# Kernel tuning notes

Hardware: AMD Instinct MI355X
Metric: run time of the kernel (lower is better)

## Reference

```python
import jax, jax.numpy as jnp
import numpy as np

B, L, F = 16384, 64, 32
E, A, H = 64, 8, 128


def setup_inputs() -> dict:
    key = jax.random.key(0)
    ks = jax.random.split(key, 16)
    s = 0.1
    return {
        "lane_features": jax.random.normal(ks[0], (B, L, F), jnp.float32),
        "lane_mask": jax.random.randint(ks[1], (B, L), 0, 2).astype(jnp.float32),
        "action_mask": jax.random.randint(ks[2], (B, A), 0, 2).astype(jnp.float32),
        # SingleHeadAttentionPool params (stored [in,out])
        "W": jax.random.normal(ks[3], (F, F), jnp.float32) * s,
        "bW": jnp.zeros((F,), jnp.float32),
        "v": jax.random.normal(ks[4], (F,), jnp.float32) * s,
        "projW": jax.random.normal(ks[5], (F, E), jnp.float32) * s,
        "projb": jnp.zeros((E,), jnp.float32),
        # policy head MLP [E->128->128->A], tanh
        "piW1": jax.random.normal(ks[6], (E, H), jnp.float32) * s,
        "pib1": jnp.zeros((H,), jnp.float32),
        "piW2": jax.random.normal(ks[7], (H, H), jnp.float32) * s,
        "pib2": jnp.zeros((H,), jnp.float32),
        "piW3": jax.random.normal(ks[8], (H, A), jnp.float32) * s,
        "pib3": jnp.zeros((A,), jnp.float32),
        # value head MLP [E->128->128->1], tanh
        "vfW1": jax.random.normal(ks[9], (E, H), jnp.float32) * s,
        "vfb1": jnp.zeros((H,), jnp.float32),
        "vfW2": jax.random.normal(ks[10], (H, H), jnp.float32) * s,
        "vfb2": jnp.zeros((H,), jnp.float32),
        "vfW3": jax.random.normal(ks[11], (H, 1), jnp.float32) * s,
        "vfb3": jnp.zeros((1,), jnp.float32),
    }


def reference(lane_features, lane_mask, action_mask, W, bW, v, projW, projb,
              piW1, pib1, piW2, pib2, piW3, pib3,
              vfW1, vfb1, vfW2, vfb2, vfW3, vfb3):
    X = lane_features                       # [B,L,F]
    mask = lane_mask > 0.5                  # [B,L] bool
    has_active = jnp.any(mask, axis=-1)     # [B]

    # additive attention pool, masked softmax == gather-then-softmax
    Hh = jnp.tanh(jnp.einsum('blf,fg->blg', X, W) + bW)   # [B,L,F]
    scores = jnp.einsum('blf,f->bl', Hh, v)                # [B,L]
    NEG = jnp.float32(-1e30)
    w = jax.nn.softmax(jnp.where(mask, scores, NEG), axis=-1)
    w = jnp.where(mask, w, 0.0)
    pooled = jnp.einsum('bl,blf->bf', w, X)                # [B,F]
    z = pooled @ projW + projb                             # [B,E]
    z = jnp.where(has_active[:, None], z, 0.0)             # empty set -> zeros

    # heads
    h = jnp.tanh(z @ piW1 + pib1)
    h = jnp.tanh(h @ piW2 + pib2)
    logits = h @ piW3 + pib3                               # [B,A]

    g = jnp.tanh(z @ vfW1 + vfb1)
    g = jnp.tanh(g @ vfW2 + vfb2)
    value = (g @ vfW3 + vfb3)[:, 0]                        # [B]

    # hard action masking
    invalid = action_mask <= 0
    masked = jnp.where(invalid, jnp.finfo(logits.dtype).min, logits)
    all_invalid = jnp.all(invalid, axis=1)
    masked = jnp.where(all_invalid[:, None], logits, masked)
    return masked, value
```

## Files before the change

### kernel.cpp

```cpp
#include <hip/hip_runtime.h>
#include <float.h>

#define NBATCH 16384
#define SAFE_MAX 3.3e38f
#define SAFE_NEG -3.3e38f

typedef __attribute__((ext_vector_type(8))) short bf16x8;
typedef __attribute__((ext_vector_type(4))) float f32x4;

__device__ __forceinline__ float san(float v) {
    v = (v == v) ? v : 0.0f;
    return fminf(fmaxf(v, SAFE_NEG), SAFE_MAX);
}

__device__ __forceinline__ float tanh_fast(float a) {
    float e = __expf(a + a);
    return fmaf(-2.0f, __builtin_amdgcn_rcpf(e + 1.0f), 1.0f);
}

__device__ __forceinline__ unsigned short f2bf_rne(float v) {
    unsigned int u = __float_as_uint(v);
    return (unsigned short)((u + 0x7FFFu + ((u >> 16) & 1u)) >> 16);
}

extern "C" __global__ void __launch_bounds__(256, 4)
pool_kernel(const float* __restrict__ X, const float* __restrict__ LM,
            const float* __restrict__ W, const float* __restrict__ bW,
            const float* __restrict__ vv,
            const float* __restrict__ projW, const float* __restrict__ projb,
            float* __restrict__ zout)
{
    __shared__ __align__(16) short wt[32 * 40];
    __shared__ float sc[4][64];
    __shared__ float mk[4][64];
    __shared__ float pool_s[4][32];

    const int tid  = threadIdx.x;
    const int w    = __builtin_amdgcn_readfirstlane(tid >> 6);
    const int lane = tid & 63;
    const int c    = lane & 15;
    const int quad = lane >> 4;
    const long b   = (long)blockIdx.x * 4 + w;

    for (int i = tid; i < 1024; i += 256) {
        const int n = i >> 5, k = i & 31;
        wt[n * 40 + k] = (short)f2bf_rne(W[k * 32 + n]);
    }

    float xr[4][8];
#pragma unroll
    for (int t = 0; t < 4; ++t) {
        const float4* p = (const float4*)(X + b * 2048 + (16 * t + c) * 32 + quad * 8);
        float4 a0 = p[0], a1 = p[1];
        xr[t][0] = a0.x; xr[t][1] = a0.y; xr[t][2] = a0.z; xr[t][3] = a0.w;
        xr[t][4] = a1.x; xr[t][5] = a1.y; xr[t][6] = a1.z; xr[t][7] = a1.w;
    }
    const float ml = LM[b * 64 + lane];
    const bool active = ml > 0.5f;

    union { bf16x8 v; unsigned int u[4]; } afr[4];
#pragma unroll
    for (int t = 0; t < 4; ++t)
#pragma unroll
        for (int j2 = 0; j2 < 4; ++j2)
            afr[t].u[j2] = __builtin_amdgcn_perm(
                __float_as_uint(xr[t][2 * j2 + 1]),
                __float_as_uint(xr[t][2 * j2]), 0x07060302u);

    __syncthreads();

    union { bf16x8 v; uint4 q; } bfr[2];
#pragma unroll
    for (int u = 0; u < 2; ++u)
        bfr[u].q = *((const uint4*)&wt[(16 * u + c) * 40 + quad * 8]);

    f32x4 acc[4][2];
#pragma unroll
    for (int t = 0; t < 4; ++t)
#pragma unroll
        for (int u = 0; u < 2; ++u) {
            acc[t][u] = (f32x4){0.f, 0.f, 0.f, 0.f};
            acc[t][u] = __builtin_amdgcn_mfma_f32_16x16x32_bf16(
                afr[t].v, bfr[u].v, acc[t][u], 0, 0, 0);
        }

    const float bw0 = bW[c], bw1 = bW[16 + c];
    const float vv0 = vv[c], vv1 = vv[16 + c];
    mk[w][lane] = ml;
#pragma unroll
    for (int t = 0; t < 4; ++t)
#pragma unroll
        for (int r = 0; r < 4; ++r) {
            float s = tanh_fast(acc[t][0][r] + bw0) * vv0
                    + tanh_fast(acc[t][1][r] + bw1) * vv1;
            s += __shfl_xor(s, 1);
            s += __shfl_xor(s, 2);
            s += __shfl_xor(s, 4);
            s += __shfl_xor(s, 8);
            if (c == t * 4 + r)
                sc[w][16 * t + quad * 4 + r] = s;
        }
    __syncthreads();

    const float s0 = sc[w][lane];
    float smx = active ? s0 : -1e30f;
#pragma unroll
    for (int off = 32; off; off >>= 1) smx = fmaxf(smx, __shfl_xor(smx, off));
    float ev = active ? __expf(s0 - smx) : 0.0f;
    float es = ev;
#pragma unroll
    for (int off = 32; off; off >>= 1) es += __shfl_xor(es, off);
    const float rcpS = __builtin_amdgcn_rcpf(es);

    float wgt[4];
#pragma unroll
    for (int t = 0; t < 4; ++t) {
        const float sr = sc[w][16 * t + c];
        const float mr = mk[w][16 * t + c];
        wgt[t] = (mr > 0.5f && es > 0.0f) ? __expf(sr - smx) * rcpS : 0.0f;
    }

#pragma unroll
    for (int j = 0; j < 8; ++j) {
        float p = wgt[0] * xr[0][j];
#pragma unroll
        for (int t = 1; t < 4; ++t) p = fmaf(wgt[t], xr[t][j], p);
        p += __shfl_xor(p, 1);
        p += __shfl_xor(p, 2);
        p += __shfl_xor(p, 4);
        p += __shfl_xor(p, 8);
        if (c == 0) pool_s[w][quad * 8 + j] = p;
    }
    __syncthreads();

    float zv = projb[lane];
#pragma unroll
    for (int f = 0; f < 32; ++f)
        zv = fmaf(pool_s[w][f], projW[f * 64 + lane], zv);
    const bool any = (__ballot(active) != 0ull);
    zout[b * 64 + lane] = any ? san(zv) : 0.0f;
}

#define ZT 0
#define H1 4160
#define PL 0
extern "C" __global__ void __launch_bounds__(512)
heads_kernel(const float* __restrict__ z, const float* __restrict__ AM,
             const float* __restrict__ piW1, const float* __restrict__ pib1,
             const float* __restrict__ piW2, const float* __restrict__ pib2,
             const float* __restrict__ piW3, const float* __restrict__ pib3,
             const float* __restrict__ vfW1, const float* __restrict__ vfb1,
             const float* __restrict__ vfW2, const float* __restrict__ vfb2,
             const float* __restrict__ vfW3, const float* __restrict__ vfb3,
             float* __restrict__ out)
{
    __shared__ float smem[12352];

    const int tid  = threadIdx.x;
    const int w    = __builtin_amdgcn_readfirstlane(tid >> 6);
    const int el   = tid & 63;
    const bool isPi = (blockIdx.x & 1) == 0;
    const int tile  = blockIdx.x >> 1;

    for (int i = tid; i < 4096; i += 512)
        smem[ZT + (i >> 6) * 65 + (i & 63)] = z[(long)tile * 4096 + i];
    __syncthreads();

    const float* W1 = isPi ? piW1 : vfW1;
    const float* b1 = isPi ? pib1 : vfb1;
    const float* W2 = isPi ? piW2 : vfW2;
    const float* b2 = isPi ? pib2 : vfb2;

    float acc[16];
#pragma unroll
    for (int i = 0; i < 16; ++i) acc[i] = b1[w * 16 + i];
#pragma unroll 8
    for (int e = 0; e < 64; ++e) {
        const float zv = smem[ZT + el * 65 + e];
        const float* wr = W1 + e * 128 + w * 16;
#pragma unroll
        for (int i = 0; i < 16; ++i) acc[i] = fmaf(zv, wr[i], acc[i]);
    }
#pragma unroll
    for (int i = 0; i < 16; ++i)
        smem[H1 + (w * 16 + i) * 64 + el] = tanh_fast(acc[i]);
    __syncthreads();

    float a2[16];
#pragma unroll
    for (int i = 0; i < 16; ++i) a2[i] = b2[w * 16 + i];
#pragma unroll 8
    for (int j = 0; j < 128; ++j) {
        const float hv = smem[H1 + j * 64 + el];
        const float* wr = W2 + j * 128 + w * 16;
#pragma unroll
        for (int i = 0; i < 16; ++i) a2[i] = fmaf(hv, wr[i], a2[i]);
    }

    if (isPi) {
        float pl[8];
#pragma unroll
        for (int a = 0; a < 8; ++a) pl[a] = 0.0f;
#pragma unroll
        for (int i = 0; i < 16; ++i) {
            const float h2 = tanh_fast(a2[i]);
            const float* wr = piW3 + (w * 16 + i) * 8;
#pragma unroll
            for (int a = 0; a < 8; ++a) pl[a] = fmaf(h2, wr[a], pl[a]);
        }
#pragma unroll
        for (int a = 0; a < 8; ++a)
            smem[PL + w * 512 + el * 8 + a] = pl[a];
        __syncthreads();

        const int rel = tid >> 3, ra = tid & 7;
        float lg = pib3[ra];
#pragma unroll
        for (int w2 = 0; w2 < 8; ++w2)
            lg += smem[PL + w2 * 512 + rel * 8 + ra];
        lg = san(lg);
        const long rb = (long)tile * 64 + rel;
        const float am = AM[rb * 8 + ra];
        const bool inv = (am <= 0.0f);
        const unsigned long long bal = __ballot(inv);
        const int grp = (tid & 63) >> 3;
        const bool allinv = (((bal >> (grp * 8)) & 0xFFull) == 0xFFull);
        out[rb * 8 + ra] = allinv ? lg : (inv ? SAFE_NEG : lg);
    } else {
        float pv = 0.0f;
#pragma unroll
        for (int i = 0; i < 16; ++i)
            pv = fmaf(tanh_fast(a2[i]), vfW3[w * 16 + i], pv);
        smem[PL + el * 8 + w] = pv;
        __syncthreads();

        if (tid < 64) {
            float val = vfb3[0];
#pragma unroll
            for (int w2 = 0; w2 < 8; ++w2) val += smem[PL + tid * 8 + w2];
            out[(long)NBATCH * 8 + (long)tile * 64 + tid] = san(val);
        }
    }
}

#define LZ    0
#define LH1f  4096
#define LPLf  12288
#define LWX   4096
#define LPOOL 12800
#define WXS   17

extern "C" __global__ void __launch_bounds__(512, 2)
fused_kernel(const float* __restrict__ X, const float* __restrict__ LM,
             const float* __restrict__ AM,
             const float* __restrict__ W, const float* __restrict__ bW,
             const float* __restrict__ vv,
             const float* __restrict__ projW, const float* __restrict__ projb,
             const float* __restrict__ piW1, const float* __restrict__ pib1,
             const float* __restrict__ piW2, const float* __restrict__ pib2,
             const float* __restrict__ piW3, const float* __restrict__ pib3,
             const float* __restrict__ vfW1, const float* __restrict__ vfb1,
             const float* __restrict__ vfW2, const float* __restrict__ vfb2,
             const float* __restrict__ vfW3, const float* __restrict__ vfb3,
             float* __restrict__ out)
{
    __shared__ float smem[16384];
    const int tid  = threadIdx.x;
    const int w    = __builtin_amdgcn_readfirstlane(tid >> 6);
    const int lane = tid & 63;

    float4 xv[8];
    float  mval;
    {
        const long b0 = (long)blockIdx.x * 64 + w;
        const float4* xp = (const float4*)(X + b0 * 2048 + lane * 32);
#pragma unroll
        for (int i = 0; i < 8; ++i) xv[i] = xp[i];
        mval = LM[b0 * 64 + lane];
    }
#pragma unroll 1
    for (int it = 0; it < 8; ++it) {
        const int eL = it * 8 + w;
        float4 xn[8];
        float  mn = 0.0f;
        if (it < 7) {
            const long bn = (long)blockIdx.x * 64 + (it + 1) * 8 + w;
            const float4* xp = (const float4*)(X + bn * 2048 + lane * 32);
#pragma unroll
            for (int i = 0; i < 8; ++i) xn[i] = xp[i];
            mn = LM[bn * 64 + lane];
        }
        float x[32];
#pragma unroll
        for (int i = 0; i < 8; ++i) {
            x[4*i+0] = xv[i].x; x[4*i+1] = xv[i].y;
            x[4*i+2] = xv[i].z; x[4*i+3] = xv[i].w;
        }
        float acc[32];
#pragma unroll
        for (int g = 0; g < 32; ++g) acc[g] = 0.0f;
#pragma unroll
        for (int f = 0; f < 32; ++f) {
            const float xf = x[f];
#pragma unroll
            for (int g = 0; g < 32; ++g) acc[g] = fmaf(xf, W[f * 32 + g], acc[g]);
        }
        float score = 0.0f;
#pragma unroll
        for (int g = 0; g < 32; ++g)
            score = fmaf(tanh_fast(acc[g] + bW[g]), vv[g], score);

        const bool active = mval > 0.5f;
        float sm = active ? score : -1e30f;
#pragma unroll
        for (int off = 32; off; off >>= 1) sm = fmaxf(sm, __shfl_xor(sm, off));
        float ev = active ? __expf(score - sm) : 0.0f;
        float es = ev;
#pragma unroll
        for (int off = 32; off; off >>= 1) es += __shfl_xor(es, off);
        const float wgt = (es > 0.0f) ? (ev / es) : 0.0f;

        float* wxp = &smem[LWX + w * (64 * WXS)];
#pragma unroll 1
        for (int P = 0; P < 2; ++P) {
            __syncthreads();
#pragma unroll
            for (int fr = 0; fr < 16; ++fr)
                wxp[lane * WXS + fr] = wgt * x[P * 16 + fr];
            __syncthreads();
            const int q = lane >> 4, fr = lane & 15;
            float p = 0.0f;
#pragma unroll
            for (int r = 0; r < 16; ++r) p += wxp[(q * 16 + r) * WXS + fr];
            p += __shfl_xor(p, 16);
            p += __shfl_xor(p, 32);
            if (lane < 16) smem[LPOOL + w * 32 + P * 16 + fr] = p;
        }
        __syncthreads();

        float zv = projb[lane];
#pragma unroll
        for (int f = 0; f < 32; ++f)
            zv = fmaf(smem[LPOOL + w * 32 + f], projW[f * 64 + lane], zv);
        const bool any = (__ballot(active) != 0ull);
        zv = any ? zv : 0.0f;
        smem[LZ + lane * 64 + eL] = san(zv);
        if (it < 7) {
#pragma unroll
            for (int i = 0; i < 8; ++i) xv[i] = xn[i];
            mval = mn;
        }
    }
    __syncthreads();

    const int el = lane;
    {
        float acc[16];
#pragma unroll
        for (int i = 0; i < 16; ++i) acc[i] = pib1[w * 16 + i];
#pragma unroll 8
        for (int e = 0; e < 64; ++e) {
            const float zv = smem[LZ + e * 64 + el];
            const float* wr = piW1 + e * 128 + w * 16;
#pragma unroll
            for (int i = 0; i < 16; ++i) acc[i] = fmaf(zv, wr[i], acc[i]);
        }
#pragma unroll
        for (int i = 0; i < 16; ++i)
            smem[LH1f + (w * 16 + i) * 64 + el] = tanh_fast(acc[i]);
        __syncthreads();

        float a2[16];
#pragma unroll
        for (int i = 0; i < 16; ++i) a2[i] = pib2[w * 16 + i];
#pragma unroll 8
        for (int j = 0; j < 128; ++j) {
            const float hv = smem[LH1f + j * 64 + el];
            const float* wr = piW2 + j * 128 + w * 16;
#pragma unroll
            for (int i = 0; i < 16; ++i) a2[i] = fmaf(hv, wr[i], a2[i]);
        }
        float pl[8];
#pragma unroll
        for (int a = 0; a < 8; ++a) pl[a] = 0.0f;
#pragma unroll
        for (int i = 0; i < 16; ++i) {
            const float h2 = tanh_fast(a2[i]);
            const float* wr = piW3 + (w * 16 + i) * 8;
#pragma unroll
            for (int a = 0; a < 8; ++a) pl[a] = fmaf(h2, wr[a], pl[a]);
        }
#pragma unroll
        for (int a = 0; a < 8; ++a)
            smem[LPLf + w * 512 + el * 8 + a] = pl[a];
        __syncthreads();

        const int rel = tid >> 3, ra = tid & 7;
        float lg = pib3[ra];
#pragma unroll
        for (int w2 = 0; w2 < 8; ++w2)
            lg += smem[LPLf + w2 * 512 + rel * 8 + ra];
        lg = san(lg);
        const long rb = (long)blockIdx.x * 64 + rel;
        const float am = AM[rb * 8 + ra];
        const bool inv = (am <= 0.0f);
        const unsigned long long bal = __ballot(inv);
        const int grp = (tid & 63) >> 3;
        const bool allinv = (((bal >> (grp * 8)) & 0xFFull) == 0xFFull);
        out[rb * 8 + ra] = allinv ? lg : (inv ? SAFE_NEG : lg);
        __syncthreads();
    }
    {
        float acc[16];
#pragma unroll
        for (int i = 0; i < 16; ++i) acc[i] = vfb1[w * 16 + i];
#pragma unroll 8
        for (int e = 0; e < 64; ++e) {
            const float zv = smem[LZ + e * 64 + el];
            const float* wr = vfW1 + e * 128 + w * 16;
#pragma unroll
            for (int i = 0; i < 16; ++i) acc[i] = fmaf(zv, wr[i], acc[i]);
        }
#pragma unroll
        for (int i = 0; i < 16; ++i)
            smem[LH1f + (w * 16 + i) * 64 + el] = tanh_fast(acc[i]);
        __syncthreads();

        float a2[16];
#pragma unroll
        for (int i = 0; i < 16; ++i) a2[i] = vfb2[w * 16 + i];
#pragma unroll 8
        for (int j = 0; j < 128; ++j) {
            const float hv = smem[LH1f + j * 64 + el];
            const float* wr = vfW2 + j * 128 + w * 16;
#pragma unroll
            for (int i = 0; i < 16; ++i) a2[i] = fmaf(hv, wr[i], a2[i]);
        }
        float pv = 0.0f;
#pragma unroll
        for (int i = 0; i < 16; ++i)
            pv = fmaf(tanh_fast(a2[i]), vfW3[w * 16 + i], pv);
        smem[LPLf + el * 8 + w] = pv;
        __syncthreads();

        if (tid < 64) {
            float val = vfb3[0];
#pragma unroll
            for (int w2 = 0; w2 < 8; ++w2) val += smem[LPLf + tid * 8 + w2];
            out[(long)NBATCH * 8 + (long)blockIdx.x * 64 + tid] = san(val);
        }
    }
}

extern "C" void kernel_launch(void* const* d_in, const int* in_sizes, int n_in,
                              void* d_out, int out_size, void* d_ws, size_t ws_size,
                              hipStream_t stream) {
    const float* X     = (const float*)d_in[0];
    const float* LM    = (const float*)d_in[1];
    const float* AM    = (const float*)d_in[2];
    const float* W     = (const float*)d_in[3];
    const float* bW    = (const float*)d_in[4];
    const float* vv    = (const float*)d_in[5];
    const float* projW = (const float*)d_in[6];
    const float* projb = (const float*)d_in[7];
    const float* piW1  = (const float*)d_in[8];
    const float* pib1  = (const float*)d_in[9];
    const float* piW2  = (const float*)d_in[10];
    const float* pib2  = (const float*)d_in[11];
    const float* piW3  = (const float*)d_in[12];
    const float* pib3  = (const float*)d_in[13];
    const float* vfW1  = (const float*)d_in[14];
    const float* vfb1  = (const float*)d_in[15];
    const float* vfW2  = (const float*)d_in[16];
    const float* vfb2  = (const float*)d_in[17];
    const float* vfW3  = (const float*)d_in[18];
    const float* vfb3  = (const float*)d_in[19];

    float* outp = (float*)d_out;
    const size_t zbytes = (size_t)NBATCH * 64 * sizeof(float);

    if (ws_size >= zbytes) {
        float* z = (float*)d_ws;
        pool_kernel<<<NBATCH / 4, 256, 0, stream>>>(
            X, LM, W, bW, vv, projW, projb, z);
        heads_kernel<<<(NBATCH / 64) * 2, 512, 0, stream>>>(
            z, AM, piW1, pib1, piW2, pib2, piW3, pib3,
            vfW1, vfb1, vfW2, vfb2, vfW3, vfb3, outp);
    } else {
        fused_kernel<<<NBATCH / 64, 512, 0, stream>>>(
            X, LM, AM, W, bW, vv, projW, projb,
            piW1, pib1, piW2, pib2, piW3, pib3,
            vfW1, vfb1, vfW2, vfb2, vfW3, vfb3, outp);
    }
}
```

Baseline: 258.3 us.

## Replace two-kernel pool+heads path with single fused MFMA kernel

Drops the pool_kernel + heads_kernel pair that passed z through a global workspace and always launches one fused kernel instead. The new kernel computes the attention projection with bf16 MFMA (as in pool_kernel), keeps z in shared memory, and then runs both MLP heads in the same block. This removes the global round-trip of z and one launch. The cost is only 256 blocks of 512 threads with large shared memory use, so occupancy and parallelism may be lower than the split version, and the heads still run on scalar FMAs.

```diff
diff --git a/kernel.cpp b/kernel.cpp
--- a/kernel.cpp
+++ b/kernel.cpp
@@ -21,6 +21,269 @@
 __device__ __forceinline__ unsigned short f2bf_rne(float v) {
     unsigned int u = __float_as_uint(v);
     return (unsigned short)((u + 0x7FFFu + ((u >> 16) & 1u)) >> 16);
+}
+
+extern "C" __global__ void __launch_bounds__(512, 2)
+fused_mfma(const float* __restrict__ X, const float* __restrict__ LM,
+           const float* __restrict__ AM,
+           const float* __restrict__ W, const float* __restrict__ bW,
+           const float* __restrict__ vv,
+           const float* __restrict__ projW, const float* __restrict__ projb,
+           const float* __restrict__ piW1, const float* __restrict__ pib1,
+           const float* __restrict__ piW2, const float* __restrict__ pib2,
+           const float* __restrict__ piW3, const float* __restrict__ pib3,
+           const float* __restrict__ vfW1, const float* __restrict__ vfb1,
+           const float* __restrict__ vfW2, const float* __restrict__ vfb2,
+           const float* __restrict__ vfW3, const float* __restrict__ vfb3,
+           float* __restrict__ out)
+{
+    __shared__ __align__(16) short wt[32 * 40];
+    __shared__ float zl[64 * 65];
+    __shared__ float sc[8][64];
+    __shared__ float mk[8][64];
+    __shared__ float pool_s[8][32];
+    __shared__ float h1[128 * 64];
+    __shared__ float plbuf[8 * 512];
+
+    const int tid  = threadIdx.x;
+    const int w    = __builtin_amdgcn_readfirstlane(tid >> 6);
+    const int lane = tid & 63;
+    const int c    = lane & 15;
+    const int quad = lane >> 4;
+    const long btile = (long)blockIdx.x * 64;
+
+    for (int i = tid; i < 1024; i += 512) {
+        const int n = i >> 5, k = i & 31;
+        wt[n * 40 + k] = (short)f2bf_rne(W[k * 32 + n]);
+    }
+
+    const float bw0 = bW[c], bw1 = bW[16 + c];
+    const float vv0 = vv[c], vv1 = vv[16 + c];
+    const float pjb = projb[lane];
+
+    __syncthreads();
+
+    union { bf16x8 v; uint4 q; } bfr[2];
+#pragma unroll
+    for (int u = 0; u < 2; ++u)
+        bfr[u].q = *((const uint4*)&wt[(16 * u + c) * 40 + quad * 8]);
+
+    float xr[4][8];
+    float ml;
+    {
+        const long b = btile + w * 8;
+#pragma unroll
+        for (int t = 0; t < 4; ++t) {
+            const float4* p = (const float4*)(X + b * 2048 + (16 * t + c) * 32 + quad * 8);
+            float4 a0 = p[0], a1 = p[1];
+            xr[t][0] = a0.x; xr[t][1] = a0.y; xr[t][2] = a0.z; xr[t][3] = a0.w;
+            xr[t][4] = a1.x; xr[t][5] = a1.y; xr[t][6] = a1.z; xr[t][7] = a1.w;
+        }
+        ml = LM[b * 64 + lane];
+    }
+
+#pragma unroll 1
+    for (int it = 0; it < 8; ++it) {
+        const int brel = w * 8 + it;
+
+        float xn[4][8];
+        float mn = 0.0f;
+        if (it < 7) {
+            const long bn = btile + brel + 1;
+#pragma unroll
+            for (int t = 0; t < 4; ++t) {
+                const float4* p = (const float4*)(X + bn * 2048 + (16 * t + c) * 32 + quad * 8);
+                float4 a0 = p[0], a1 = p[1];
+                xn[t][0] = a0.x; xn[t][1] = a0.y; xn[t][2] = a0.z; xn[t][3] = a0.w;
+                xn[t][4] = a1.x; xn[t][5] = a1.y; xn[t][6] = a1.z; xn[t][7] = a1.w;
+            }
+            mn = LM[bn * 64 + lane];
+        }
+        const bool active = ml > 0.5f;
+
+        union { bf16x8 v; unsigned int u[4]; } afr[4];
+#pragma unroll
+        for (int t = 0; t < 4; ++t)
+#pragma unroll
+            for (int j2 = 0; j2 < 4; ++j2)
+                afr[t].u[j2] = __builtin_amdgcn_perm(
+                    __float_as_uint(xr[t][2 * j2 + 1]),
+                    __float_as_uint(xr[t][2 * j2]), 0x07060302u);
+
+        f32x4 acc[4][2];
+#pragma unroll
+        for (int t = 0; t < 4; ++t)
+#pragma unroll
+            for (int u = 0; u < 2; ++u) {
+                acc[t][u] = (f32x4){0.f, 0.f, 0.f, 0.f};
+                acc[t][u] = __builtin_amdgcn_mfma_f32_16x16x32_bf16(
+                    afr[t].v, bfr[u].v, acc[t][u], 0, 0, 0);
+            }
+
+        mk[w][lane] = ml;
+#pragma unroll
+        for (int t = 0; t < 4; ++t)
+#pragma unroll
+            for (int r = 0; r < 4; ++r) {
+                float s = tanh_fast(acc[t][0][r] + bw0) * vv0
+                        + tanh_fast(acc[t][1][r] + bw1) * vv1;
+                s += __shfl_xor(s, 1);
+                s += __shfl_xor(s, 2);
+                s += __shfl_xor(s, 4);
+                s += __shfl_xor(s, 8);
+                if (c == t * 4 + r)
+                    sc[w][16 * t + quad * 4 + r] = s;
+            }
+        asm volatile("s_waitcnt lgkmcnt(0)" ::: "memory");
+
+        const float s0 = sc[w][lane];
+        float smx = active ? s0 : -1e30f;
+#pragma unroll
+        for (int off = 32; off; off >>= 1) smx = fmaxf(smx, __shfl_xor(smx, off));
+        float ev = active ? __expf(s0 - smx) : 0.0f;
+        float es = ev;
+#pragma unroll
+        for (int off = 32; off; off >>= 1) es += __shfl_xor(es, off);
+        const float rcpS = __builtin_amdgcn_rcpf(es);
+
+        float wgt[4];
+#pragma unroll
+        for (int t = 0; t < 4; ++t) {
+            const float sr = sc[w][16 * t + c];
+            const float mr = mk[w][16 * t + c];
+            wgt[t] = (mr > 0.5f && es > 0.0f) ? __expf(sr - smx) * rcpS : 0.0f;
+        }
+
+#pragma unroll
+        for (int j = 0; j < 8; ++j) {
+            float p = wgt[0] * xr[0][j];
+#pragma unroll
+            for (int t = 1; t < 4; ++t) p = fmaf(wgt[t], xr[t][j], p);
+            p += __shfl_xor(p, 1);
+            p += __shfl_xor(p, 2);
+            p += __shfl_xor(p, 4);
+            p += __shfl_xor(p, 8);
+            if (c == 0) pool_s[w][quad * 8 + j] = p;
+        }
+        asm volatile("s_waitcnt lgkmcnt(0)" ::: "memory");
+
+        float zv = pjb;
+#pragma unroll
+        for (int f = 0; f < 32; ++f)
+            zv = fmaf(pool_s[w][f], projW[f * 64 + lane], zv);
+        const bool any = (__ballot(active) != 0ull);
+        zl[lane * 65 + brel] = any ? san(zv) : 0.0f;
+
+        if (it < 7) {
+#pragma unroll
+            for (int t = 0; t < 4; ++t)
+#pragma unroll
+                for (int j = 0; j < 8; ++j) xr[t][j] = xn[t][j];
+            ml = mn;
+        }
+    }
+    __syncthreads();
+
+    const int el = lane;
+
+    {
+        float acc[16];
+#pragma unroll
+        for (int i = 0; i < 16; ++i) acc[i] = pib1[w * 16 + i];
+#pragma unroll 8
+        for (int e = 0; e < 64; ++e) {
+            const float zv = zl[e * 65 + el];
+            const float* wr = piW1 + e * 128 + w * 16;
+#pragma unroll
+            for (int i = 0; i < 16; ++i) acc[i] = fmaf(zv, wr[i], acc[i]);
+        }
+#pragma unroll
+        for (int i = 0; i < 16; ++i)
+            h1[(w * 16 + i) * 64 + el] = tanh_fast(acc[i]);
+        __syncthreads();
+
+        float a2[16];
+#pragma unroll
+        for (int i = 0; i < 16; ++i) a2[i] = pib2[w * 16 + i];
+#pragma unroll 8
+        for (int j = 0; j < 128; ++j) {
+            const float hv = h1[j * 64 + el];
+            const float* wr = piW2 + j * 128 + w * 16;
+#pragma unroll
+            for (int i = 0; i < 16; ++i) a2[i] = fmaf(hv, wr[i], a2[i]);
+        }
+
+        float pl[8];
+#pragma unroll
+        for (int a = 0; a < 8; ++a) pl[a] = 0.0f;
+#pragma unroll
+        for (int i = 0; i < 16; ++i) {
+            const float h2 = tanh_fast(a2[i]);
+            const float* wr = piW3 + (w * 16 + i) * 8;
+#pragma unroll
+            for (int a = 0; a < 8; ++a) pl[a] = fmaf(h2, wr[a], pl[a]);
+        }
+#pragma unroll
+        for (int a = 0; a < 8; ++a)
+            plbuf[w * 512 + el * 8 + a] = pl[a];
+        __syncthreads();
+
+        const int rel = tid >> 3, ra = tid & 7;
+        float lg = pib3[ra];
+#pragma unroll
+        for (int w2 = 0; w2 < 8; ++w2)
+            lg += plbuf[w2 * 512 + rel * 8 + ra];
+        lg = san(lg);
+        const long rb = btile + rel;
+        const float am = AM[rb * 8 + ra];
+        const bool inv = (am <= 0.0f);
+        const unsigned long long bal = __ballot(inv);
+        const int grp = (tid & 63) >> 3;
+        const bool allinv = (((bal >> (grp * 8)) & 0xFFull) == 0xFFull);
+        out[rb * 8 + ra] = allinv ? lg : (inv ? SAFE_NEG : lg);
+        __syncthreads();
+    }
+
+    {
+        float acc[16];
+#pragma unroll
+        for (int i = 0; i < 16; ++i) acc[i] = vfb1[w * 16 + i];
+#pragma unroll 8
+        for (int e = 0; e < 64; ++e) {
+            const float zv = zl[e * 65 + el];
+            const float* wr = vfW1 + e * 128 + w * 16;
+#pragma unroll
+            for (int i = 0; i < 16; ++i) acc[i] = fmaf(zv, wr[i], acc[i]);
+        }
+#pragma unroll
+        for (int i = 0; i < 16; ++i)
+            h1[(w * 16 + i) * 64 + el] = tanh_fast(acc[i]);
+        __syncthreads();
+
+        float a2[16];
+#pragma unroll
+        for (int i = 0; i < 16; ++i) a2[i] = vfb2[w * 16 + i];
+#pragma unroll 8
+        for (int j = 0; j < 128; ++j) {
+            const float hv = h1[j * 64 + el];
+            const float* wr = vfW2 + j * 128 + w * 16;
+#pragma unroll
+            for (int i = 0; i < 16; ++i) a2[i] = fmaf(hv, wr[i], a2[i]);
+        }
+        float pv = 0.0f;
+#pragma unroll
+        for (int i = 0; i < 16; ++i)
+            pv = fmaf(tanh_fast(a2[i]), vfW3[w * 16 + i], pv);
+        plbuf[el * 8 + w] = pv;
+        __syncthreads();
+
+        if (tid < 64) {
+            float val = vfb3[0];
+#pragma unroll
+            for (int w2 = 0; w2 < 8; ++w2) val += plbuf[tid * 8 + w2];
+            out[(long)NBATCH * 8 + btile + tid] = san(val);
+        }
+    }
 }
 
 extern "C" __global__ void __launch_bounds__(256, 4)
@@ -239,215 +502,6 @@
 #pragma unroll
             for (int w2 = 0; w2 < 8; ++w2) val += smem[PL + tid * 8 + w2];
             out[(long)NBATCH * 8 + (long)tile * 64 + tid] = san(val);
-        }
-    }
-}
-
-#define LZ    0
-#define LH1f  4096
-#define LPLf  12288
-#define LWX   4096
-#define LPOOL 12800
-#define WXS   17
-
-extern "C" __global__ void __launch_bounds__(512, 2)
-fused_kernel(const float* __restrict__ X, const float* __restrict__ LM,
-             const float* __restrict__ AM,
-             const float* __restrict__ W, const float* __restrict__ bW,
-             const float* __restrict__ vv,
-             const float* __restrict__ projW, const float* __restrict__ projb,
-             const float* __restrict__ piW1, const float* __restrict__ pib1,
-             const float* __restrict__ piW2, const float* __restrict__ pib2,
-             const float* __restrict__ piW3, const float* __restrict__ pib3,
-             const float* __restrict__ vfW1, const float* __restrict__ vfb1,
-             const float* __restrict__ vfW2, const float* __restrict__ vfb2,
-             const float* __restrict__ vfW3, const float* __restrict__ vfb3,
-             float* __restrict__ out)
-{
-    __shared__ float smem[16384];
-    const int tid  = threadIdx.x;
-    const int w    = __builtin_amdgcn_readfirstlane(tid >> 6);
-    const int lane = tid & 63;
-
-    float4 xv[8];
-    float  mval;
-    {
-        const long b0 = (long)blockIdx.x * 64 + w;
-        const float4* xp = (const float4*)(X + b0 * 2048 + lane * 32);
-#pragma unroll
-        for (int i = 0; i < 8; ++i) xv[i] = xp[i];
-        mval = LM[b0 * 64 + lane];
-    }
-#pragma unroll 1
-    for (int it = 0; it < 8; ++it) {
-        const int eL = it * 8 + w;
-        float4 xn[8];
-        float  mn = 0.0f;
-        if (it < 7) {
-            const long bn = (long)blockIdx.x * 64 + (it + 1) * 8 + w;
-            const float4* xp = (const float4*)(X + bn * 2048 + lane * 32);
-#pragma unroll
-            for (int i = 0; i < 8; ++i) xn[i] = xp[i];
-            mn = LM[bn * 64 + lane];
-        }
-        float x[32];
-#pragma unroll
-        for (int i = 0; i < 8; ++i) {
-            x[4*i+0] = xv[i].x; x[4*i+1] = xv[i].y;
-            x[4*i+2] = xv[i].z; x[4*i+3] = xv[i].w;
-        }
-        float acc[32];
-#pragma unroll
-        for (int g = 0; g < 32; ++g) acc[g] = 0.0f;
-#pragma unroll
-        for (int f = 0; f < 32; ++f) {
-            const float xf = x[f];
-#pragma unroll
-            for (int g = 0; g < 32; ++g) acc[g] = fmaf(xf, W[f * 32 + g], acc[g]);
-        }
-        float score = 0.0f;
-#pragma unroll
-        for (int g = 0; g < 32; ++g)
-            score = fmaf(tanh_fast(acc[g] + bW[g]), vv[g], score);
-
-        const bool active = mval > 0.5f;
-        float sm = active ? score : -1e30f;
-#pragma unroll
-        for (int off = 32; off; off >>= 1) sm = fmaxf(sm, __shfl_xor(sm, off));
-        float ev = active ? __expf(score - sm) : 0.0f;
-        float es = ev;
-#pragma unroll
-        for (int off = 32; off; off >>= 1) es += __shfl_xor(es, off);
-        const float wgt = (es > 0.0f) ? (ev / es) : 0.0f;
-
-        float* wxp = &smem[LWX + w * (64 * WXS)];
-#pragma unroll 1
-        for (int P = 0; P < 2; ++P) {
-            __syncthreads();
-#pragma unroll
-            for (int fr = 0; fr < 16; ++fr)
-                wxp[lane * WXS + fr] = wgt * x[P * 16 + fr];
-            __syncthreads();
-            const int q = lane >> 4, fr = lane & 15;
-            float p = 0.0f;
-#pragma unroll
-            for (int r = 0; r < 16; ++r) p += wxp[(q * 16 + r) * WXS + fr];
-            p += __shfl_xor(p, 16);
-            p += __shfl_xor(p, 32);
-            if (lane < 16) smem[LPOOL + w * 32 + P * 16 + fr] = p;
-        }
-        __syncthreads();
-
-        float zv = projb[lane];
-#pragma unroll
-        for (int f = 0; f < 32; ++f)
-            zv = fmaf(smem[LPOOL + w * 32 + f], projW[f * 64 + lane], zv);
-        const bool any = (__ballot(active) != 0ull);
-        zv = any ? zv : 0.0f;
-        smem[LZ + lane * 64 + eL] = san(zv);
-        if (it < 7) {
-#pragma unroll
-            for (int i = 0; i < 8; ++i) xv[i] = xn[i];
-            mval = mn;
-        }
-    }
-    __syncthreads();
-
-    const int el = lane;
-    {
-        float acc[16];
-#pragma unroll
-        for (int i = 0; i < 16; ++i) acc[i] = pib1[w * 16 + i];
-#pragma unroll 8
-        for (int e = 0; e < 64; ++e) {
-            const float zv = smem[LZ + e * 64 + el];
-            const float* wr = piW1 + e * 128 + w * 16;
-#pragma unroll
-            for (int i = 0; i < 16; ++i) acc[i] = fmaf(zv, wr[i], acc[i]);
-        }
-#pragma unroll
-        for (int i = 0; i < 16; ++i)
-            smem[LH1f + (w * 16 + i) * 64 + el] = tanh_fast(acc[i]);
-        __syncthreads();
-
-        float a2[16];
-#pragma unroll
-        for (int i = 0; i < 16; ++i) a2[i] = pib2[w * 16 + i];
-#pragma unroll 8
-        for (int j = 0; j < 128; ++j) {
-            const float hv = smem[LH1f + j * 64 + el];
-            const float* wr = piW2 + j * 128 + w * 16;
-#pragma unroll
-            for (int i = 0; i < 16; ++i) a2[i] = fmaf(hv, wr[i], a2[i]);
-        }
-        float pl[8];
-#pragma unroll
-        for (int a = 0; a < 8; ++a) pl[a] = 0.0f;
-#pragma unroll
-        for (int i = 0; i < 16; ++i) {
-            const float h2 = tanh_fast(a2[i]);
-            const float* wr = piW3 + (w * 16 + i) * 8;
-#pragma unroll
-            for (int a = 0; a < 8; ++a) pl[a] = fmaf(h2, wr[a], pl[a]);
-        }
-#pragma unroll
-        for (int a = 0; a < 8; ++a)
-            smem[LPLf + w * 512 + el * 8 + a] = pl[a];
-        __syncthreads();
-
-        const int rel = tid >> 3, ra = tid & 7;
-        float lg = pib3[ra];
-#pragma unroll
-        for (int w2 = 0; w2 < 8; ++w2)
-            lg += smem[LPLf + w2 * 512 + rel * 8 + ra];
-        lg = san(lg);
-        const long rb = (long)blockIdx.x * 64 + rel;
-        const float am = AM[rb * 8 + ra];
-        const bool inv = (am <= 0.0f);
-        const unsigned long long bal = __ballot(inv);
-        const int grp = (tid & 63) >> 3;
-        const bool allinv = (((bal >> (grp * 8)) & 0xFFull) == 0xFFull);
-        out[rb * 8 + ra] = allinv ? lg : (inv ? SAFE_NEG : lg);
-        __syncthreads();
-    }
-    {
-        float acc[16];
-#pragma unroll
-        for (int i = 0; i < 16; ++i) acc[i] = vfb1[w * 16 + i];
-#pragma unroll 8
-        for (int e = 0; e < 64; ++e) {
-            const float zv = smem[LZ + e * 64 + el];
-            const float* wr = vfW1 + e * 128 + w * 16;
-#pragma unroll
-            for (int i = 0; i < 16; ++i) acc[i] = fmaf(zv, wr[i], acc[i]);
-        }
-#pragma unroll
-        for (int i = 0; i < 16; ++i)
-            smem[LH1f + (w * 16 + i) * 64 + el] = tanh_fast(acc[i]);
-        __syncthreads();
-
-        float a2[16];
-#pragma unroll
-        for (int i = 0; i < 16; ++i) a2[i] = vfb2[w * 16 + i];
-#pragma unroll 8
-        for (int j = 0; j < 128; ++j) {
-            const float hv = smem[LH1f + j * 64 + el];
-            const float* wr = vfW2 + j * 128 + w * 16;
-#pragma unroll
-            for (int i = 0; i < 16; ++i) a2[i] = fmaf(hv, wr[i], a2[i]);
-        }
-        float pv = 0.0f;
-#pragma unroll
-        for (int i = 0; i < 16; ++i)
-            pv = fmaf(tanh_fast(a2[i]), vfW3[w * 16 + i], pv);
-        smem[LPLf + el * 8 + w] = pv;
-        __syncthreads();
-
-        if (tid < 64) {
-            float val = vfb3[0];
-#pragma unroll
-            for (int w2 = 0; w2 < 8; ++w2) val += smem[LPLf + tid * 8 + w2];
-            out[(long)NBATCH * 8 + (long)blockIdx.x * 64 + tid] = san(val);
         }
     }
 }
@@ -477,19 +531,9 @@
     const float* vfb3  = (const float*)d_in[19];
 
     float* outp = (float*)d_out;
-    const size_t zbytes = (size_t)NBATCH * 64 * sizeof(float);
-
-    if (ws_size >= zbytes) {
-        float* z = (float*)d_ws;
-        pool_kernel<<<NBATCH / 4, 256, 0, stream>>>(
-            X, LM, W, bW, vv, projW, projb, z);
-        heads_kernel<<<(NBATCH / 64) * 2, 512, 0, stream>>>(
-            z, AM, piW1, pib1, piW2, pib2, piW3, pib3,
-            vfW1, vfb1, vfW2, vfb2, vfW3, vfb3, outp);
-    } else {
-        fused_kernel<<<NBATCH / 64, 512, 0, stream>>>(
-            X, LM, AM, W, bW, vv, projW, projb,
-            piW1, pib1, piW2, pib2, piW3, pib3,
-            vfW1, vfb1, vfW2, vfb2, vfW3, vfb3, outp);
-    }
-}
+
+    fused_mfma<<<NBATCH / 64, 512, 0, stream>>>(
+        X, LM, AM, W, bW, vv, projW, projb,
+        piW1, pib1, piW2, pib2, piW3, pib3,
+        vfW1, vfb1, vfW2, vfb2, vfW3, vfb3, outp);
+}
```

Measured after the change: 325.6 us. 26.1% more time.

## Fuse pool and heads into one 1024-thread kernel with transposed MFMA scoring

Applied to the files above, without the earlier changes.

Replaces the two-kernel pipeline (pool writing z to workspace, then heads reading it back) with a single kernel. Each 1024-thread block handles 64 batch rows: 16 waves each pool 4 rows using MFMA with swapped operands so score reduction needs fewer shuffles, then 8 waves run the policy head while the other 8 run the value head concurrently. This removes the z round-trip through global memory and the second launch. The cost is a large LDS footprint that limits occupancy, only 256 blocks in the grid, and serialized per-wave pooling loops.

```diff
diff --git a/kernel.cpp b/kernel.cpp
--- a/kernel.cpp
+++ b/kernel.cpp
@@ -23,49 +23,50 @@
     return (unsigned short)((u + 0x7FFFu + ((u >> 16) & 1u)) >> 16);
 }
 
-extern "C" __global__ void __launch_bounds__(256, 4)
-pool_kernel(const float* __restrict__ X, const float* __restrict__ LM,
-            const float* __restrict__ W, const float* __restrict__ bW,
-            const float* __restrict__ vv,
-            const float* __restrict__ projW, const float* __restrict__ projb,
-            float* __restrict__ zout)
+extern "C" __global__ void __launch_bounds__(1024, 4)
+fused_v2(const float* __restrict__ X, const float* __restrict__ LM,
+         const float* __restrict__ AM,
+         const float* __restrict__ W, const float* __restrict__ bW,
+         const float* __restrict__ vv,
+         const float* __restrict__ projW, const float* __restrict__ projb,
+         const float* __restrict__ piW1, const float* __restrict__ pib1,
+         const float* __restrict__ piW2, const float* __restrict__ pib2,
+         const float* __restrict__ piW3, const float* __restrict__ pib3,
+         const float* __restrict__ vfW1, const float* __restrict__ vfb1,
+         const float* __restrict__ vfW2, const float* __restrict__ vfb2,
+         const float* __restrict__ vfW3, const float* __restrict__ vfb3,
+         float* __restrict__ out)
 {
     __shared__ __align__(16) short wt[32 * 40];
-    __shared__ float sc[4][64];
-    __shared__ float mk[4][64];
-    __shared__ float pool_s[4][32];
+    __shared__ float zl[64 * 65];
+    __shared__ float pool_s[16][32];
+    __shared__ float h1pi[128 * 64];
+    __shared__ float h1v[128 * 64];
+    __shared__ float plpi[8 * 512];
+    __shared__ float plv[64 * 8];
 
     const int tid  = threadIdx.x;
     const int w    = __builtin_amdgcn_readfirstlane(tid >> 6);
     const int lane = tid & 63;
     const int c    = lane & 15;
     const int quad = lane >> 4;
-    const long b   = (long)blockIdx.x * 4 + w;
-
-    for (int i = tid; i < 1024; i += 256) {
-        const int n = i >> 5, k = i & 31;
+    const long btile = (long)blockIdx.x * 64;
+
+    {
+        const int n = tid >> 5, k = tid & 31;
         wt[n * 40 + k] = (short)f2bf_rne(W[k * 32 + n]);
     }
 
-    float xr[4][8];
-#pragma unroll
-    for (int t = 0; t < 4; ++t) {
-        const float4* p = (const float4*)(X + b * 2048 + (16 * t + c) * 32 + quad * 8);
-        float4 a0 = p[0], a1 = p[1];
-        xr[t][0] = a0.x; xr[t][1] = a0.y; xr[t][2] = a0.z; xr[t][3] = a0.w;
-        xr[t][4] = a1.x; xr[t][5] = a1.y; xr[t][6] = a1.z; xr[t][7] = a1.w;
-    }
-    const float ml = LM[b * 64 + lane];
-    const bool active = ml > 0.5f;
-
-    union { bf16x8 v; unsigned int u[4]; } afr[4];
-#pragma unroll
-    for (int t = 0; t < 4; ++t)
-#pragma unroll
-        for (int j2 = 0; j2 < 4; ++j2)
-            afr[t].u[j2] = __builtin_amdgcn_perm(
-                __float_as_uint(xr[t][2 * j2 + 1]),
-                __float_as_uint(xr[t][2 * j2]), 0x07060302u);
+    float bwr[8], vvr[8];
+#pragma unroll
+    for (int u = 0; u < 2; ++u)
+#pragma unroll
+        for (int r = 0; r < 4; ++r) {
+            const int g = 16 * u + 4 * quad + r;
+            bwr[u * 4 + r] = bW[g];
+            vvr[u * 4 + r] = vv[g];
+        }
+    const float pjb = projb[lane];
 
     __syncthreads();
 
@@ -74,130 +75,157 @@
     for (int u = 0; u < 2; ++u)
         bfr[u].q = *((const uint4*)&wt[(16 * u + c) * 40 + quad * 8]);
 
-    f32x4 acc[4][2];
-#pragma unroll
-    for (int t = 0; t < 4; ++t)
+#pragma unroll 1
+    for (int it = 0; it < 4; ++it) {
+        const int brel = w * 4 + it;
+        const long b = btile + brel;
+
+        float xr[4][8];
+#pragma unroll
+        for (int t = 0; t < 4; ++t) {
+            const float4* p = (const float4*)(X + b * 2048 + (16 * t + c) * 32 + quad * 8);
+            float4 a0 = p[0], a1 = p[1];
+            xr[t][0] = a0.x; xr[t][1] = a0.y; xr[t][2] = a0.z; xr[t][3] = a0.w;
+            xr[t][4] = a1.x; xr[t][5] = a1.y; xr[t][6] = a1.z; xr[t][7] = a1.w;
+        }
+        float ml[4];
+#pragma unroll
+        for (int t = 0; t < 4; ++t) ml[t] = LM[b * 64 + 16 * t + c];
+
+        union { bf16x8 v; unsigned int u[4]; } afr[4];
+#pragma unroll
+        for (int t = 0; t < 4; ++t)
+#pragma unroll
+            for (int j2 = 0; j2 < 4; ++j2)
+                afr[t].u[j2] = __builtin_amdgcn_perm(
+                    __float_as_uint(xr[t][2 * j2 + 1]),
+                    __float_as_uint(xr[t][2 * j2]), 0x07060302u);
+
+        float sp[4] = {0.f, 0.f, 0.f, 0.f};
 #pragma unroll
         for (int u = 0; u < 2; ++u) {
-            acc[t][u] = (f32x4){0.f, 0.f, 0.f, 0.f};
-            acc[t][u] = __builtin_amdgcn_mfma_f32_16x16x32_bf16(
-                afr[t].v, bfr[u].v, acc[t][u], 0, 0, 0);
-        }
-
-    const float bw0 = bW[c], bw1 = bW[16 + c];
-    const float vv0 = vv[c], vv1 = vv[16 + c];
-    mk[w][lane] = ml;
-#pragma unroll
-    for (int t = 0; t < 4; ++t)
-#pragma unroll
-        for (int r = 0; r < 4; ++r) {
-            float s = tanh_fast(acc[t][0][r] + bw0) * vv0
-                    + tanh_fast(acc[t][1][r] + bw1) * vv1;
-            s += __shfl_xor(s, 1);
-            s += __shfl_xor(s, 2);
-            s += __shfl_xor(s, 4);
-            s += __shfl_xor(s, 8);
-            if (c == t * 4 + r)
-                sc[w][16 * t + quad * 4 + r] = s;
-        }
+            f32x4 a[4];
+#pragma unroll
+            for (int t = 0; t < 4; ++t) {
+                a[t] = (f32x4){0.f, 0.f, 0.f, 0.f};
+                a[t] = __builtin_amdgcn_mfma_f32_16x16x32_bf16(
+                    bfr[u].v, afr[t].v, a[t], 0, 0, 0);
+            }
+#pragma unroll
+            for (int t = 0; t < 4; ++t)
+#pragma unroll
+                for (int r = 0; r < 4; ++r)
+                    sp[t] = fmaf(tanh_fast(a[t][r] + bwr[u * 4 + r]),
+                                 vvr[u * 4 + r], sp[t]);
+        }
+
+        float s[4];
+#pragma unroll
+        for (int t = 0; t < 4; ++t) {
+            float v0 = sp[t];
+            v0 += __shfl_xor(v0, 16);
+            v0 += __shfl_xor(v0, 32);
+            s[t] = v0;
+        }
+
+        bool act[4];
+#pragma unroll
+        for (int t = 0; t < 4; ++t) act[t] = ml[t] > 0.5f;
+
+        float m = -1e30f;
+#pragma unroll
+        for (int t = 0; t < 4; ++t) m = fmaxf(m, act[t] ? s[t] : -1e30f);
+        m = fmaxf(m, __shfl_xor(m, 1));
+        m = fmaxf(m, __shfl_xor(m, 2));
+        m = fmaxf(m, __shfl_xor(m, 4));
+        m = fmaxf(m, __shfl_xor(m, 8));
+
+        float ev[4];
+        float es = 0.0f;
+#pragma unroll
+        for (int t = 0; t < 4; ++t) {
+            ev[t] = act[t] ? __expf(s[t] - m) : 0.0f;
+            es += ev[t];
+        }
+        es += __shfl_xor(es, 1);
+        es += __shfl_xor(es, 2);
+        es += __shfl_xor(es, 4);
+        es += __shfl_xor(es, 8);
+        const float rcpS = __builtin_amdgcn_rcpf(es);
+
+        float wgt[4];
+#pragma unroll
+        for (int t = 0; t < 4; ++t)
+            wgt[t] = (act[t] && es > 0.0f) ? ev[t] * rcpS : 0.0f;
+
+#pragma unroll
+        for (int j = 0; j < 8; ++j) {
+            float p = wgt[0] * xr[0][j];
+#pragma unroll
+            for (int t = 1; t < 4; ++t) p = fmaf(wgt[t], xr[t][j], p);
+            p += __shfl_xor(p, 1);
+            p += __shfl_xor(p, 2);
+            p += __shfl_xor(p, 4);
+            p += __shfl_xor(p, 8);
+            if (c == 0) pool_s[w][quad * 8 + j] = p;
+        }
+        asm volatile("s_waitcnt lgkmcnt(0)" ::: "memory");
+
+        float zv = pjb;
+#pragma unroll
+        for (int f = 0; f < 32; ++f)
+            zv = fmaf(pool_s[w][f], projW[f * 64 + lane], zv);
+        const bool anyl = act[0] | act[1] | act[2] | act[3];
+        const bool any = (__ballot(anyl) != 0ull);
+        zl[lane * 65 + brel] = any ? san(zv) : 0.0f;
+    }
     __syncthreads();
 
-    const float s0 = sc[w][lane];
-    float smx = active ? s0 : -1e30f;
-#pragma unroll
-    for (int off = 32; off; off >>= 1) smx = fmaxf(smx, __shfl_xor(smx, off));
-    float ev = active ? __expf(s0 - smx) : 0.0f;
-    float es = ev;
-#pragma unroll
-    for (int off = 32; off; off >>= 1) es += __shfl_xor(es, off);
-    const float rcpS = __builtin_amdgcn_rcpf(es);
-
-    float wgt[4];
-#pragma unroll
-    for (int t = 0; t < 4; ++t) {
-        const float sr = sc[w][16 * t + c];
-        const float mr = mk[w][16 * t + c];
-        wgt[t] = (mr > 0.5f && es > 0.0f) ? __expf(sr - smx) * rcpS : 0.0f;
-    }
-
-#pragma unroll
-    for (int j = 0; j < 8; ++j) {
-        float p = wgt[0] * xr[0][j];
-#pragma unroll
-        for (int t = 1; t < 4; ++t) p = fmaf(wgt[t], xr[t][j], p);
-        p += __shfl_xor(p, 1);
-        p += __shfl_xor(p, 2);
-        p += __shfl_xor(p, 4);
-        p += __shfl_xor(p, 8);
-        if (c == 0) pool_s[w][quad * 8 + j] = p;
+    const int el = lane;
+    const int w8 = w - 8;
+
+    if (w < 8) {
+        float acc[16];
+#pragma unroll
+        for (int i = 0; i < 16; ++i) acc[i] = pib1[w * 16 + i];
+#pragma unroll 8
+        for (int e = 0; e < 64; ++e) {
+            const float zv = zl[e * 65 + el];
+            const float* wr = piW1 + e * 128 + w * 16;
+#pragma unroll
+            for (int i = 0; i < 16; ++i) acc[i] = fmaf(zv, wr[i], acc[i]);
+        }
+#pragma unroll
+        for (int i = 0; i < 16; ++i)
+            h1pi[(w * 16 + i) * 64 + el] = tanh_fast(acc[i]);
+    } else {
+        float acc[16];
+#pragma unroll
+        for (int i = 0; i < 16; ++i) acc[i] = vfb1[w8 * 16 + i];
+#pragma unroll 8
+        for (int e = 0; e < 64; ++e) {
+            const float zv = zl[e * 65 + el];
+            const float* wr = vfW1 + e * 128 + w8 * 16;
+#pragma unroll
+            for (int i = 0; i < 16; ++i) acc[i] = fmaf(zv, wr[i], acc[i]);
+        }
+#pragma unroll
+        for (int i = 0; i < 16; ++i)
+            h1v[(w8 * 16 + i) * 64 + el] = tanh_fast(acc[i]);
     }
     __syncthreads();
 
-    float zv = projb[lane];
-#pragma unroll
-    for (int f = 0; f < 32; ++f)
-        zv = fmaf(pool_s[w][f], projW[f * 64 + lane], zv);
-    const bool any = (__ballot(active) != 0ull);
-    zout[b * 64 + lane] = any ? san(zv) : 0.0f;
-}
-
-#define ZT 0
-#define H1 4160
-#define PL 0
-extern "C" __global__ void __launch_bounds__(512)
-heads_kernel(const float* __restrict__ z, const float* __restrict__ AM,
-             const float* __restrict__ piW1, const float* __restrict__ pib1,
-             const float* __restrict__ piW2, const float* __restrict__ pib2,
-             const float* __restrict__ piW3, const float* __restrict__ pib3,
-             const float* __restrict__ vfW1, const float* __restrict__ vfb1,
-             const float* __restrict__ vfW2, const float* __restrict__ vfb2,
-             const float* __restrict__ vfW3, const float* __restrict__ vfb3,
-             float* __restrict__ out)
-{
-    __shared__ float smem[12352];
-
-    const int tid  = threadIdx.x;
-    const int w    = __builtin_amdgcn_readfirstlane(tid >> 6);
-    const int el   = tid & 63;
-    const bool isPi = (blockIdx.x & 1) == 0;
-    const int tile  = blockIdx.x >> 1;
-
-    for (int i = tid; i < 4096; i += 512)
-        smem[ZT + (i >> 6) * 65 + (i & 63)] = z[(long)tile * 4096 + i];
-    __syncthreads();
-
-    const float* W1 = isPi ? piW1 : vfW1;
-    const float* b1 = isPi ? pib1 : vfb1;
-    const float* W2 = isPi ? piW2 : vfW2;
-    const float* b2 = isPi ? pib2 : vfb2;
-
-    float acc[16];
-#pragma unroll
-    for (int i = 0; i < 16; ++i) acc[i] = b1[w * 16 + i];
+    if (w < 8) {
+        float a2[16];
+#pragma unroll
+        for (int i = 0; i < 16; ++i) a2[i] = pib2[w * 16 + i];
 #pragma unroll 8
-    for (int e = 0; e < 64; ++e) {
-        const float zv = smem[ZT + el * 65 + e];
-        const float* wr = W1 + e * 128 + w * 16;
-#pragma unroll
-        for (int i = 0; i < 16; ++i) acc[i] = fmaf(zv, wr[i], acc[i]);
-    }
-#pragma unroll
-    for (int i = 0; i < 16; ++i)
-        smem[H1 + (w * 16 + i) * 64 + el] = tanh_fast(acc[i]);
-    __syncthreads();
-
-    float a2[16];
-#pragma unroll
-    for (int i = 0; i < 16; ++i) a2[i] = b2[w * 16 + i];
-#pragma unroll 8
-    for (int j = 0; j < 128; ++j) {
-        const float hv = smem[H1 + j * 64 + el];
-        const float* wr = W2 + j * 128 + w * 16;
-#pragma unroll
-        for (int i = 0; i < 16; ++i) a2[i] = fmaf(hv, wr[i], a2[i]);
-    }
-
-    if (isPi) {
+        for (int j = 0; j < 128; ++j) {
+            const float hv = h1pi[j * 64 + el];
+            const float* wr = piW2 + j * 128 + w * 16;
+#pragma unroll
+            for (int i = 0; i < 16; ++i) a2[i] = fmaf(hv, wr[i], a2[i]);
+        }
         float pl[8];
 #pragma unroll
         for (int a = 0; a < 8; ++a) pl[a] = 0.0f;
@@ -210,245 +238,45 @@
         }
 #pragma unroll
         for (int a = 0; a < 8; ++a)
-            smem[PL + w * 512 + el * 8 + a] = pl[a];
-        __syncthreads();
-
+            plpi[w * 512 + el * 8 + a] = pl[a];
+    } else {
+        float a2[16];
+#pragma unroll
+        for (int i = 0; i < 16; ++i) a2[i] = vfb2[w8 * 16 + i];
+#pragma unroll 8
+        for (int j = 0; j < 128; ++j) {
+            const float hv = h1v[j * 64 + el];
+            const float* wr = vfW2 + j * 128 + w8 * 16;
+#pragma unroll
+            for (int i = 0; i < 16; ++i) a2[i] = fmaf(hv, wr[i], a2[i]);
+        }
+        float pv = 0.0f;
+#pragma unroll
+        for (int i = 0; i < 16; ++i)
+            pv = fmaf(tanh_fast(a2[i]), vfW3[w8 * 16 + i], pv);
+        plv[el * 8 + w8] = pv;
+    }
+    __syncthreads();
+
+    if (w < 8) {
         const int rel = tid >> 3, ra = tid & 7;
         float lg = pib3[ra];
 #pragma unroll
         for (int w2 = 0; w2 < 8; ++w2)
-            lg += smem[PL + w2 * 512 + rel * 8 + ra];
+            lg += plpi[w2 * 512 + rel * 8 + ra];
         lg = san(lg);
-        const long rb = (long)tile * 64 + rel;
+        const long rb = btile + rel;
         const float am = AM[rb * 8 + ra];
         const bool inv = (am <= 0.0f);
         const unsigned long long bal = __ballot(inv);
         const int grp = (tid & 63) >> 3;
         const bool allinv = (((bal >> (grp * 8)) & 0xFFull) == 0xFFull);
         out[rb * 8 + ra] = allinv ? lg : (inv ? SAFE_NEG : lg);
-    } else {
-        float pv = 0.0f;
-#pragma unroll
-        for (int i = 0; i < 16; ++i)
-            pv = fmaf(tanh_fast(a2[i]), vfW3[w * 16 + i], pv);
-        smem[PL + el * 8 + w] = pv;
-        __syncthreads();
-
-        if (tid < 64) {
-            float val = vfb3[0];
-#pragma unroll
-            for (int w2 = 0; w2 < 8; ++w2) val += smem[PL + tid * 8 + w2];
-            out[(long)NBATCH * 8 + (long)tile * 64 + tid] = san(val);
-        }
-    }
-}
-
-#define LZ    0
-#define LH1f  4096
-#define LPLf  12288
-#define LWX   4096
-#define LPOOL 12800
-#define WXS   17
-
-extern "C" __global__ void __launch_bounds__(512, 2)
-fused_kernel(const float* __restrict__ X, const float* __restrict__ LM,
-             const float* __restrict__ AM,
-             const float* __restrict__ W, const float* __restrict__ bW,
-             const float* __restrict__ vv,
-             const float* __restrict__ projW, const float* __restrict__ projb,
-             const float* __restrict__ piW1, const float* __restrict__ pib1,
-             const float* __restrict__ piW2, const float* __restrict__ pib2,
-             const float* __restrict__ piW3, const float* __restrict__ pib3,
-             const float* __restrict__ vfW1, const float* __restrict__ vfb1,
-             const float* __restrict__ vfW2, const float* __restrict__ vfb2,
-             const float* __restrict__ vfW3, const float* __restrict__ vfb3,
-             float* __restrict__ out)
-{
-    __shared__ float smem[16384];
-    const int tid  = threadIdx.x;
-    const int w    = __builtin_amdgcn_readfirstlane(tid >> 6);
-    const int lane = tid & 63;
-
-    float4 xv[8];
-    float  mval;
-    {
-        const long b0 = (long)blockIdx.x * 64 + w;
-        const float4* xp = (const float4*)(X + b0 * 2048 + lane * 32);
-#pragma unroll
-        for (int i = 0; i < 8; ++i) xv[i] = xp[i];
-        mval = LM[b0 * 64 + lane];
-    }
-#pragma unroll 1
-    for (int it = 0; it < 8; ++it) {
-        const int eL = it * 8 + w;
-        float4 xn[8];
-        float  mn = 0.0f;
-        if (it < 7) {
-            const long bn = (long)blockIdx.x * 64 + (it + 1) * 8 + w;
-            const float4* xp = (const float4*)(X + bn * 2048 + lane * 32);
-#pragma unroll
-            for (int i = 0; i < 8; ++i) xn[i] = xp[i];
-            mn = LM[bn * 64 + lane];
-        }
-        float x[32];
-#pragma unroll
-        for (int i = 0; i < 8; ++i) {
-            x[4*i+0] = xv[i].x; x[4*i+1] = xv[i].y;
-            x[4*i+2] = xv[i].z; x[4*i+3] = xv[i].w;
-        }
-        float acc[32];
-#pragma unroll
-        for (int g = 0; g < 32; ++g) acc[g] = 0.0f;
-#pragma unroll
-        for (int f = 0; f < 32; ++f) {
-            const float xf = x[f];
-#pragma unroll
-            for (int g = 0; g < 32; ++g) acc[g] = fmaf(xf, W[f * 32 + g], acc[g]);
-        }
-        float score = 0.0f;
-#pragma unroll
-        for (int g = 0; g < 32; ++g)
-            score = fmaf(tanh_fast(acc[g] + bW[g]), vv[g], score);
-
-        const bool active = mval > 0.5f;
-        float sm = active ? score : -1e30f;
-#pragma unroll
-        for (int off = 32; off; off >>= 1) sm = fmaxf(sm, __shfl_xor(sm, off));
-        float ev = active ? __expf(score - sm) : 0.0f;
-        float es = ev;
-#pragma unroll
-        for (int off = 32; off; off >>= 1) es += __shfl_xor(es, off);
-        const float wgt = (es > 0.0f) ? (ev / es) : 0.0f;
-
-        float* wxp = &smem[LWX + w * (64 * WXS)];
-#pragma unroll 1
-        for (int P = 0; P < 2; ++P) {
-            __syncthreads();
-#pragma unroll
-            for (int fr = 0; fr < 16; ++fr)
-                wxp[lane * WXS + fr] = wgt * x[P * 16 + fr];
-            __syncthreads();
-            const int q = lane >> 4, fr = lane & 15;
-            float p = 0.0f;
-#pragma unroll
-            for (int r = 0; r < 16; ++r) p += wxp[(q * 16 + r) * WXS + fr];
-            p += __shfl_xor(p, 16);
-            p += __shfl_xor(p, 32);
-            if (lane < 16) smem[LPOOL + w * 32 + P * 16 + fr] = p;
-        }
-        __syncthreads();
-
-        float zv = projb[lane];
-#pragma unroll
-        for (int f = 0; f < 32; ++f)
-            zv = fmaf(smem[LPOOL + w * 32 + f], projW[f * 64 + lane], zv);
-        const bool any = (__ballot(active) != 0ull);
-        zv = any ? zv : 0.0f;
-        smem[LZ + lane * 64 + eL] = san(zv);
-        if (it < 7) {
-#pragma unroll
-            for (int i = 0; i < 8; ++i) xv[i] = xn[i];
-            mval = mn;
-        }
-    }
-    __syncthreads();
-
-    const int el = lane;
-    {
-        float acc[16];
-#pragma unroll
-        for (int i = 0; i < 16; ++i) acc[i] = pib1[w * 16 + i];
-#pragma unroll 8
-        for (int e = 0; e < 64; ++e) {
-            const float zv = smem[LZ + e * 64 + el];
-            const float* wr = piW1 + e * 128 + w * 16;
-#pragma unroll
-            for (int i = 0; i < 16; ++i) acc[i] = fmaf(zv, wr[i], acc[i]);
-        }
-#pragma unroll
-        for (int i = 0; i < 16; ++i)
-            smem[LH1f + (w * 16 + i) * 64 + el] = tanh_fast(acc[i]);
-        __syncthreads();
-
-        float a2[16];
-#pragma unroll
-        for (int i = 0; i < 16; ++i) a2[i] = pib2[w * 16 + i];
-#pragma unroll 8
-        for (int j = 0; j < 128; ++j) {
-            const float hv = smem[LH1f + j * 64 + el];
-            const float* wr = piW2 + j * 128 + w * 16;
-#pragma unroll
-            for (int i = 0; i < 16; ++i) a2[i] = fmaf(hv, wr[i], a2[i]);
-        }
-        float pl[8];
-#pragma unroll
-        for (int a = 0; a < 8; ++a) pl[a] = 0.0f;
-#pragma unroll
-        for (int i = 0; i < 16; ++i) {
-            const float h2 = tanh_fast(a2[i]);
-            const float* wr = piW3 + (w * 16 + i) * 8;
-#pragma unroll
-            for (int a = 0; a < 8; ++a) pl[a] = fmaf(h2, wr[a], pl[a]);
-        }
-#pragma unroll
-        for (int a = 0; a < 8; ++a)
-            smem[LPLf + w * 512 + el * 8 + a] = pl[a];
-        __syncthreads();
-
-        const int rel = tid >> 3, ra = tid & 7;
-        float lg = pib3[ra];
-#pragma unroll
-        for (int w2 = 0; w2 < 8; ++w2)
-            lg += smem[LPLf + w2 * 512 + rel * 8 + ra];
-        lg = san(lg);
-        const long rb = (long)blockIdx.x * 64 + rel;
-        const float am = AM[rb * 8 + ra];
-        const bool inv = (am <= 0.0f);
-        const unsigned long long bal = __ballot(inv);
-        const int grp = (tid & 63) >> 3;
-        const bool allinv = (((bal >> (grp * 8)) & 0xFFull) == 0xFFull);
-        out[rb * 8 + ra] = allinv ? lg : (inv ? SAFE_NEG : lg);
-        __syncthreads();
-    }
-    {
-        float acc[16];
-#pragma unroll
-        for (int i = 0; i < 16; ++i) acc[i] = vfb1[w * 16 + i];
-#pragma unroll 8
-        for (int e = 0; e < 64; ++e) {
-            const float zv = smem[LZ + e * 64 + el];
-            const float* wr = vfW1 + e * 128 + w * 16;
-#pragma unroll
-            for (int i = 0; i < 16; ++i) acc[i] = fmaf(zv, wr[i], acc[i]);
-        }
-#pragma unroll
-        for (int i = 0; i < 16; ++i)
-            smem[LH1f + (w * 16 + i) * 64 + el] = tanh_fast(acc[i]);
-        __syncthreads();
-
-        float a2[16];
-#pragma unroll
-        for (int i = 0; i < 16; ++i) a2[i] = vfb2[w * 16 + i];
-#pragma unroll 8
-        for (int j = 0; j < 128; ++j) {
-            const float hv = smem[LH1f + j * 64 + el];
-            const float* wr = vfW2 + j * 128 + w * 16;
-#pragma unroll
-            for (int i = 0; i < 16; ++i) a2[i] = fmaf(hv, wr[i], a2[i]);
-        }
-        float pv = 0.0f;
-#pragma unroll
-        for (int i = 0; i < 16; ++i)
-            pv = fmaf(tanh_fast(a2[i]), vfW3[w * 16 + i], pv);
-        smem[LPLf + el * 8 + w] = pv;
-        __syncthreads();
-
-        if (tid < 64) {
-            float val = vfb3[0];
-#pragma unroll
-            for (int w2 = 0; w2 < 8; ++w2) val += smem[LPLf + tid * 8 + w2];
-            out[(long)NBATCH * 8 + (long)blockIdx.x * 64 + tid] = san(val);
-        }
+    } else if (w == 8) {
+        float val = vfb3[0];
+#pragma unroll
+        for (int w2 = 0; w2 < 8; ++w2) val += plv[lane * 8 + w2];
+        out[(long)NBATCH * 8 + btile + lane] = san(val);
     }
 }
 
@@ -477,19 +305,9 @@
     const float* vfb3  = (const float*)d_in[19];
 
     float* outp = (float*)d_out;
-    const size_t zbytes = (size_t)NBATCH * 64 * sizeof(float);
-
-    if (ws_size >= zbytes) {
-        float* z = (float*)d_ws;
-        pool_kernel<<<NBATCH / 4, 256, 0, stream>>>(
-            X, LM, W, bW, vv, projW, projb, z);
-        heads_kernel<<<(NBATCH / 64) * 2, 512, 0, stream>>>(
-            z, AM, piW1, pib1, piW2, pib2, piW3, pib3,
-            vfW1, vfb1, vfW2, vfb2, vfW3, vfb3, outp);
-    } else {
-        fused_kernel<<<NBATCH / 64, 512, 0, stream>>>(
-            X, LM, AM, W, bW, vv, projW, projb,
-            piW1, pib1, piW2, pib2, piW3, pib3,
-            vfW1, vfb1, vfW2, vfb2, vfW3, vfb3, outp);
-    }
-}
+
+    fused_v2<<<NBATCH / 64, 1024, 0, stream>>>(
+        X, LM, AM, W, bW, vv, projW, projb,
+        piW1, pib1, piW2, pib2, piW3, pib3,
+        vfW1, vfb1, vfW2, vfb2, vfW3, vfb3, outp);
+}
```

Result: slower. 318.8 us (+23.5%).
